# Optimization experiments

Measured on AMD Instinct MI355X. Metric: run time of the kernel, lower is better.

The kernel has to match this reference:

```python
import jax, jax.numpy as jnp
import numpy as np
import math

B, T, DIN, DOUT, D, L, H = 32, 512, 263, 263, 1024, 8, 16
EPS = 1e-5


def layer_norm(x, g, b):
    mu = jnp.mean(x, axis=-1, keepdims=True)
    var = jnp.var(x, axis=-1, keepdims=True)
    return (x - mu) * jax.lax.rsqrt(var + EPS) * g + b


def setup_inputs() -> dict:
    key = jax.random.key(0)
    ks = jax.random.split(key, 12)
    s = 0.02
    return {
        "x": jax.random.normal(ks[0], (B, T, DIN), jnp.float32),
        "src_mask": jnp.ones((B, T, T), jnp.bool_),
        "seq_emb": jax.random.normal(ks[1], (T, D), jnp.float32),  # sequence_embedding[:T]
        "joint_w": jax.random.normal(ks[2], (D, DIN), jnp.float32) * s,
        "joint_b": jnp.zeros((D,), jnp.float32),
        "ln_g": jnp.ones((L, D), jnp.float32),
        "ln_b": jnp.zeros((L, D), jnp.float32),
        "q_w": jax.random.normal(ks[3], (L, D, D), jnp.float32) * s,
        "q_b": jnp.zeros((L, D), jnp.float32),
        "k_w": jax.random.normal(ks[4], (L, D, D), jnp.float32) * s,
        "k_b": jnp.zeros((L, D), jnp.float32),
        "v_w": jax.random.normal(ks[5], (L, D, D), jnp.float32) * s,
        "v_b": jnp.zeros((L, D), jnp.float32),
        "p_w": jax.random.normal(ks[6], (L, D, D), jnp.float32) * s,
        "p_b": jnp.zeros((L, D), jnp.float32),
        "out_ln_g": jnp.ones((D,), jnp.float32),
        "out_ln_b": jnp.zeros((D,), jnp.float32),
        "out_w": jax.random.normal(ks[7], (DOUT, D), jnp.float32) * s,  # zero_module in ckpt; random here for non-degenerate baseline
        "out_b": jnp.zeros((DOUT,), jnp.float32),
    }


def reference(x, src_mask, seq_emb, joint_w, joint_b, ln_g, ln_b,
              q_w, q_b, k_w, k_b, v_w, v_b, p_w, p_b,
              out_ln_g, out_ln_b, out_w, out_b):
    Bc, Tc, _ = x.shape
    h = x @ joint_w.T + joint_b + seq_emb[None, :Tc, :]  # [B,T,D]
    neg = (1.0 - src_mask.astype(h.dtype))[..., None] * -100000.0  # [B,T,T,1]
    scale = 1.0 / math.sqrt(D // H)
    for i in range(L):
        n = layer_norm(h, ln_g[i], ln_b[i])
        q = (n @ q_w[i].T + q_b[i]).reshape(Bc, Tc, H, D // H)
        k = (n @ k_w[i].T + k_b[i]).reshape(Bc, Tc, H, D // H)
        v = (n @ v_w[i].T + v_b[i]).reshape(Bc, Tc, H, D // H)
        att = jnp.einsum('bnhd,bmhd->bnmh', q, k) * scale + neg
        w = jax.nn.softmax(att, axis=2)  # softmax over keys (m)
        y = jnp.einsum('bnmh,bmhd->bnhd', w, v).reshape(Bc, Tc, D)
        h = h + y @ p_w[i].T + p_b[i]
    return layer_norm(h, out_ln_g, out_ln_b) @ out_w.T + out_b
```

## Files before the change

### kernel.cpp

```cpp
#include <hip/hip_runtime.h>
#include <hip/hip_bf16.h>


typedef unsigned short u16;
typedef unsigned int u32;
typedef __attribute__((ext_vector_type(8))) __bf16 bf16x8;
typedef __attribute__((ext_vector_type(4))) float floatx4;
typedef __attribute__((ext_vector_type(4))) _Float16 halfx4;
typedef __attribute__((ext_vector_type(8))) _Float16 halfx8;

#define TB 512
#define DB 1024
#define F32_ONE 0x3F800000u
#define ATTN_SCALE 0.18033688f

__device__ __forceinline__ float bf2f(u16 u) { union { u32 i; float f; } c; c.i = ((u32)u) << 16; return c.f; }
__device__ __forceinline__ u16 f2bf(float f) {
  union { float f; u32 i; } c; c.f = f;
  return (u16)((c.i + 0x7fffu + ((c.i >> 16) & 1u)) >> 16);
}
__device__ __forceinline__ u32 pk_f16(float a, float b) {
  auto h = __builtin_amdgcn_cvt_pkrtz(a, b);
  union { decltype(h) v; u32 u; } c;
  c.v = h;
  return c.u;
}

__device__ __forceinline__ void gload16(const u16* g, u16* l) {
  __builtin_amdgcn_global_load_lds((const __attribute__((address_space(1))) void*)g,
                                   (__attribute__((address_space(3))) void*)l, 16, 0, 0);
}

__device__ __forceinline__ floatx4 mfma_pv(u32 p0, u32 p1, halfx4 vf, floatx4 c) {
#if __has_builtin(__builtin_amdgcn_mfma_f32_16x16x16f16)
  union { u32 u[2]; halfx4 h; } a; a.u[0] = p0; a.u[1] = p1;
  return __builtin_amdgcn_mfma_f32_16x16x16f16(a.h, vf, c, 0, 0, 0);
#else
  union { u32 u[4]; halfx8 h; } a; a.u[0] = p0; a.u[1] = p1; a.u[2] = 0; a.u[3] = 0;
  union { u32 u[4]; halfx8 h; halfx4 v4[2]; } b; b.u[2] = 0; b.u[3] = 0; b.v4[0] = vf;
  return __builtin_amdgcn_mfma_f32_16x16x32_f16(a.h, b.h, c, 0, 0, 0);
#endif
}

__global__ void cvt_bf16(const void* __restrict__ src, unsigned long long soff,
                         u16* __restrict__ dst, int rows_src, int cols_src,
                         int rows_dst, int cols_dst, const u32* __restrict__ det) {
  const bool isf = (det[0] == F32_ONE);
  const int idx = blockIdx.x * 256 + threadIdx.x;
  if (idx >= rows_dst * cols_dst) return;
  const int r = idx / cols_dst, c = idx - r * cols_dst;
  u16 v = 0;
  if (r < rows_src && c < cols_src) {
    const unsigned long long si = soff + (unsigned long long)r * cols_src + c;
    v = isf ? f2bf(((const float*)src)[si]) : ((const u16*)src)[si];
  }
  dst[idx] = v;
}

__global__ void cvt_f32(const void* __restrict__ src, float* __restrict__ dst,
                        int n_src, int n_dst, const u32* __restrict__ det) {
  const bool isf = (det[0] == F32_ONE);
  const int idx = blockIdx.x * 256 + threadIdx.x;
  if (idx >= n_dst) return;
  float v = 0.f;
  if (idx < n_src) v = isf ? ((const float*)src)[idx] : bf2f(((const u16*)src)[idx]);
  dst[idx] = v;
}

__global__ void cvt_wqkvp(const void* __restrict__ qw, const void* __restrict__ kw,
                          const void* __restrict__ vw, const void* __restrict__ pw,
                          unsigned long long woff, u16* __restrict__ dst,
                          const u32* __restrict__ det) {
  const bool isf = (det[0] == F32_ONE);
  const int idx = blockIdx.x * 256 + threadIdx.x;
  const int t = idx >> 20;
  const unsigned long long si = woff + (unsigned long long)(idx & 1048575);
  const void* src = (t == 0) ? qw : (t == 1) ? kw : (t == 2) ? vw : pw;
  dst[idx] = isf ? f2bf(((const float*)src)[si]) : ((const u16*)src)[si];
}

struct SmallTab {
  const void* src[10];
  float* dst[10];
  int nsrc[10];
  int ndst[10];
  int blk0[11];
};
__global__ void cvt_small(SmallTab tab, const u32* __restrict__ det) {
  const bool isf = (det[0] == F32_ONE);
  int s = 0;
  while (s < 9 && (int)blockIdx.x >= tab.blk0[s + 1]) ++s;
  const int idx = ((int)blockIdx.x - tab.blk0[s]) * 256 + threadIdx.x;
  if (idx >= tab.ndst[s]) return;
  float v = 0.f;
  if (idx < tab.nsrc[s])
    v = isf ? ((const float*)tab.src[s])[idx] : bf2f(((const u16*)tab.src[s])[idx]);
  tab.dst[s][idx] = v;
}

template <int MODE>
__global__ __launch_bounds__(256, 2) void gemm_bt(
    const u16* __restrict__ A, const u16* __restrict__ W,
    const float* __restrict__ bias, const float* __restrict__ bias2,
    const float* __restrict__ bias3,
    int M, int N, int K, int nbx,
    u16* __restrict__ Cbf, u16* __restrict__ Vtb, float* __restrict__ Hres,
    const float* __restrict__ seqf, void* __restrict__ Cout, int Ncol,
    const u32* __restrict__ det) {
  __shared__ u16 As[4096];
  __shared__ u16 Bs[4096];
  const int tid = threadIdx.x;
  const int lane = tid & 63;
  const int w = tid >> 6;

  const int nby = (int)gridDim.x / nbx;
  const int sby = nby >> 3;
  const int xcd = blockIdx.x & 7;
  const int lid = blockIdx.x >> 3;
  const int by = xcd * sby + (lid % sby);
  const int bx = lid / sby;
  const int m0 = by << 7;
  const int n0 = bx << 7;

  const int wm = (w >> 1) << 6;
  const int wn = (w & 1) << 6;

  const int srow = (w << 5) + (lane >> 2);
  const int koff = (lane & 3) << 3;
  const u16* Ag0 = A + (size_t)(m0 + srow) * K + koff;
  const u16* Ag1 = A + (size_t)(m0 + srow + 16) * K + koff;
  const u16* Wg0 = W + (size_t)(n0 + srow) * K + koff;
  const u16* Wg1 = W + (size_t)(n0 + srow + 16) * K + koff;
  u16* AsB0 = As + (w << 10);
  u16* AsB1 = AsB0 + 512;
  u16* BsB0 = Bs + (w << 10);
  u16* BsB1 = BsB0 + 512;

  floatx4 acc[4][4];
  floatx4 zz = {0.f, 0.f, 0.f, 0.f};
#pragma unroll
  for (int i = 0; i < 4; ++i)
#pragma unroll
    for (int j = 0; j < 4; ++j) acc[i][j] = zz;

  const int fr = lane & 15;
  const int fq = (lane >> 4) << 3;

  for (int k0 = 0; k0 < K; k0 += 32) {
    __syncthreads();
    gload16(Ag0 + k0, AsB0);
    gload16(Ag1 + k0, AsB1);
    gload16(Wg0 + k0, BsB0);
    gload16(Wg1 + k0, BsB1);
    __syncthreads();
    bf16x8 af[4], bfv[4];
#pragma unroll
    for (int i = 0; i < 4; ++i) af[i] = *(const bf16x8*)(As + ((wm + (i << 4) + fr) << 5) + fq);
#pragma unroll
    for (int j = 0; j < 4; ++j) bfv[j] = *(const bf16x8*)(Bs + ((wn + (j << 4) + fr) << 5) + fq);
#pragma unroll
    for (int i = 0; i < 4; ++i)
#pragma unroll
      for (int j = 0; j < 4; ++j)
        acc[i][j] = __builtin_amdgcn_mfma_f32_16x16x32_bf16(af[i], bfv[j], acc[i][j], 0, 0, 0);
  }

  const int er = (lane >> 4) << 2;
  const int ec = lane & 15;
  bool isf = true;
  if (MODE == 3) isf = (det[0] == F32_ONE);

#pragma unroll
  for (int i = 0; i < 4; ++i) {
#pragma unroll
    for (int j = 0; j < 4; ++j) {
      const int col = n0 + wn + (j << 4) + ec;
#pragma unroll
      for (int r = 0; r < 4; ++r) {
        const int row = m0 + wm + (i << 4) + er + r;
        float vv = acc[i][j][r];
        if (MODE == 1) {
          vv += bias[col];
          Hres[(size_t)row * N + col] += vv;
        } else if (MODE == 2) {
          vv += bias[col] + seqf[(size_t)(row & (TB - 1)) * N + col];
          Hres[(size_t)row * N + col] = vv;
        } else if (MODE == 3) {
          if (col < Ncol) {
            vv += bias[col];
            if (isf) ((float*)Cout)[(size_t)row * Ncol + col] = vv;
            else ((u16*)Cout)[(size_t)row * Ncol + col] = f2bf(vv);
          }
        }
      }
    }
  }
}


#define LGKM(n) asm volatile("s_waitcnt lgkmcnt(" #n ")" ::: "memory")

#define STAGE_A(t, h)                                                        \
  do {                                                                       \
    u16* slot_ = sh + (((t) & 1) << 15) + ((h) << 13) + (w << 9);            \
    gload16(pA[h][0] + ((t) << 6), slot_);                                   \
    gload16(pA[h][1] + ((t) << 6), slot_ + 4096);                            \
  } while (0)
#define STAGE_B(t, h)                                                        \
  do {                                                                       \
    u16* slot_ = sh + (((t) & 1) << 15) + 16384 + ((h) << 13) + (w << 9);    \
    gload16(pB[h][0] + ((t) << 6), slot_);                                   \
    gload16(pB[h][1] + ((t) << 6), slot_ + 4096);                            \
  } while (0)

#define LDA4P(DST, IG0)                                                       \
  do {                                                                        \
    _Pragma("unroll") for (int i_ = 0; i_ < 4; ++i_) {                        \
      DST[i_][0] = *(const bf16x8*)(sh + aB0 + (((IG0) + i_) << 10));         \
      DST[i_][1] = *(const bf16x8*)(sh + aB1 + (((IG0) + i_) << 10));         \
    }                                                                         \
  } while (0)
#define LDB2P(DST, JG0)                                                       \
  do {                                                                        \
    _Pragma("unroll") for (int j_ = 0; j_ < 2; ++j_) {                        \
      DST[j_][0] = *(const bf16x8*)(sh + bB0 + (((JG0) + j_) << 10));         \
      DST[j_][1] = *(const bf16x8*)(sh + bB1 + (((JG0) + j_) << 10));         \
    }                                                                         \
  } while (0)
#define MFMA16(I0, J0, AF, BB)                                                \
  do {                                                                        \
    __builtin_amdgcn_s_setprio(1);                                            \
    _Pragma("unroll") for (int i_ = 0; i_ < 4; ++i_) {                        \
      _Pragma("unroll") for (int j_ = 0; j_ < 2; ++j_) {                      \
        _Pragma("unroll") for (int ks_ = 0; ks_ < 2; ++ks_) {                 \
          acc[(I0) + i_][(J0) + j_] = __builtin_amdgcn_mfma_f32_16x16x32_bf16(\
              AF[i_][ks_], BB[j_][ks_], acc[(I0) + i_][(J0) + j_], 0, 0, 0);  \
        }                                                                     \
      }                                                                       \
    }                                                                         \
    __builtin_amdgcn_s_setprio(0);                                            \
  } while (0)

template <int MODE>
__global__ __launch_bounds__(512, 1) void gemm256_bt(
    const u16* __restrict__ A, const u16* __restrict__ W,
    const float* __restrict__ bias, const float* __restrict__ bias2,
    const float* __restrict__ bias3,
    int M, int N, int K, int nbx,
    u16* __restrict__ Cbf, u16* __restrict__ Vtb, float* __restrict__ Hres,
    const u32* __restrict__ det) {
  __shared__ u16 sh[65536];
  const int tid = threadIdx.x;
  const int lane = tid & 63;
  const int w = tid >> 6;

  const int nby = (int)gridDim.x / nbx;
  const int sby = nby >> 3;
  const int xcd = blockIdx.x & 7;
  const int lid = blockIdx.x >> 3;
  const int by = xcd * sby + (lid % sby);
  const int bx = lid / sby;
  const int m0 = by << 8;
  const int n0 = bx << 8;

  const int wmh = w >> 2;
  const int wnq = w & 3;
  const int wnh = wnq >> 1;
  const int wn1 = wnq & 1;

  const int fr = lane & 15;
  const int q4 = (lane >> 4) << 3;
  const int axor = (fr & 7) << 3;
  const int koff0 = q4 ^ axor;
  const int koff1 = (32 + q4) ^ axor;

  int aB0 = (wmh << 13) + (fr << 6) + koff0;
  int aB1 = (wmh << 13) + (fr << 6) + koff1;
  int bB0 = 16384 + (wnh << 13) + (wn1 << 12) + (fr << 6) + koff0;
  int bB1 = 16384 + (wnh << 13) + (wn1 << 12) + (fr << 6) + koff1;

  const int srow = (w << 3) + (lane >> 3);
  const int kbs2 = (((lane & 7) ^ (lane >> 3)) << 3);
  const u16* pA[2][2];
  const u16* pB[2][2];
#pragma unroll
  for (int h = 0; h < 2; ++h)
#pragma unroll
    for (int j = 0; j < 2; ++j) {
      pA[h][j] = A + (size_t)(m0 + (h << 7) + (j << 6) + srow) * K + kbs2;
      pB[h][j] = W + (size_t)(n0 + (h << 7) + (j << 6) + srow) * K + kbs2;
    }

  floatx4 acc[8][4];
  floatx4 zz = {0.f, 0.f, 0.f, 0.f};
#pragma unroll
  for (int i = 0; i < 8; ++i)
#pragma unroll
    for (int j = 0; j < 4; ++j) acc[i][j] = zz;

  STAGE_A(0, 0);
  STAGE_A(0, 1);
  STAGE_B(0, 0);
  STAGE_B(0, 1);
  STAGE_B(1, 0);
  STAGE_B(1, 1);
  asm volatile("s_waitcnt vmcnt(4)" ::: "memory");
  __builtin_amdgcn_s_barrier();

  bf16x8 afX[4][2], afY[4][2], b0[2][2], b1[2][2];
  const int NT = K >> 6;

  LDA4P(afX, 0);
  LDB2P(b0, 0);
  for (int t = 0; t < NT; ++t) {
    LDB2P(b1, 2);
    if (t + 1 < NT) STAGE_A(t + 1, 0);
    LGKM(4);
    MFMA16(0, 0, afX, b0);
    LDA4P(afY, 4);
    if (t + 1 < NT) STAGE_A(t + 1, 1);
    LGKM(8);
    MFMA16(0, 2, afX, b1);
    __builtin_amdgcn_s_barrier();
    if (t + 2 < NT) STAGE_B(t + 2, 0);
    LGKM(0);
    MFMA16(4, 0, afY, b0);
    if (t + 2 < NT) {
      STAGE_B(t + 2, 1);
      asm volatile("s_waitcnt vmcnt(4)" ::: "memory");
    } else {
      asm volatile("s_waitcnt vmcnt(0)" ::: "memory");
    }
    __builtin_amdgcn_s_barrier();
    aB0 ^= 32768; aB1 ^= 32768; bB0 ^= 32768; bB1 ^= 32768;
    if (t + 1 < NT) {
      LDA4P(afX, 0);
      LDB2P(b0, 0);
    }
    MFMA16(4, 2, afY, b1);
  }

  const int er = (lane >> 4) << 2;
  const int ec = lane & 15;

  if (MODE == 5 && n0 >= 2048) {
    const int colp0 = n0 - 2048;
    const int key0 = m0 & 511;
    const int bb = m0 >> 9;
#pragma unroll
    for (int p = 0; p < 2; ++p) {
      __syncthreads();
      if (wnh == p) {
#pragma unroll
        for (int i = 0; i < 8; ++i)
#pragma unroll
          for (int j = 0; j < 4; ++j) {
            const int c = (wn1 << 6) + (j << 4) + ec;
            const float bv = bias3[colp0 + (p << 7) + c];
            const int keyl = (wmh << 7) + (i << 4) + er;
            uint2 pk2;
            pk2.x = pk_f16(acc[i][j][0] + bv, acc[i][j][1] + bv);
            pk2.y = pk_f16(acc[i][j][2] + bv, acc[i][j][3] + bv);
            *(uint2*)&sh[c * 264 + keyl] = pk2;
          }
      }
      __syncthreads();
#pragma unroll
      for (int it = 0; it < 8; ++it) {
        const int idx = (it << 9) + tid;
        const int c = idx >> 5;
        const int ch = idx & 31;
        const int colp = colp0 + (p << 7) + c;
        u16* dst = Vtb + ((((size_t)((bb << 4) | (colp >> 6)) << 6) | (colp & 63)) << 9) +
                   key0 + (ch << 3);
        *(uint4*)dst = *(const uint4*)&sh[c * 264 + (ch << 3)];
      }
    }
    return;
  }

#pragma unroll
  for (int i = 0; i < 8; ++i) {
#pragma unroll
    for (int j = 0; j < 4; ++j) {
      const int col = n0 + (wnq << 6) + (j << 4) + ec;
      if (MODE == 5) {
        const float bv = (col < 1024) ? bias[col] : bias2[col - 1024];
#pragma unroll
        for (int r = 0; r < 4; ++r) {
          const int row = m0 + (wmh << 7) + (i << 4) + er + r;
          Cbf[(size_t)row * 2048 + col] = f2bf(acc[i][j][r] + bv);
        }
      } else if (MODE == 1) {
        const float bv = bias[col];
#pragma unroll
        for (int r = 0; r < 4; ++r) {
          const int row = m0 + (wmh << 7) + (i << 4) + er + r;
          Hres[(size_t)row * N + col] += acc[i][j][r] + bv;
        }
      }
    }
  }
}

__global__ __launch_bounds__(256, 4) void ln_kernel(const float* __restrict__ h,
                                                    const float* __restrict__ g,
                                                    const float* __restrict__ b,
                                                    u16* __restrict__ outp) {
  const int w = threadIdx.x >> 6, lane = threadIdx.x & 63;
  const int row = (blockIdx.x << 2) + w;
  const float4* hr = (const float4*)(h + (size_t)row * DB);
  float4 xv[4];
  float s = 0.f, ss = 0.f;
#pragma unroll
  for (int k = 0; k < 4; ++k) {
    xv[k] = hr[lane + (k << 6)];
    s += (xv[k].x + xv[k].y) + (xv[k].z + xv[k].w);
    ss += (xv[k].x * xv[k].x + xv[k].y * xv[k].y) + (xv[k].z * xv[k].z + xv[k].w * xv[k].w);
  }
#pragma unroll
  for (int o = 32; o > 0; o >>= 1) {
    s += __shfl_xor(s, o);
    ss += __shfl_xor(ss, o);
  }
  const float mu = s * (1.f / 1024.f);
  const float var = ss * (1.f / 1024.f) - mu * mu;
  const float rstd = rsqrtf(var + 1e-5f);
  u32* orow = (u32*)(outp + (size_t)row * DB);
#pragma unroll
  for (int k = 0; k < 4; ++k) {
    const float4 gv = ((const float4*)g)[lane + (k << 6)];
    const float4 bv = ((const float4*)b)[lane + (k << 6)];
    const float y0 = (xv[k].x - mu) * rstd * gv.x + bv.x;
    const float y1 = (xv[k].y - mu) * rstd * gv.y + bv.y;
    const float y2 = (xv[k].z - mu) * rstd * gv.z + bv.z;
    const float y3 = (xv[k].w - mu) * rstd * gv.w + bv.w;
    orow[((lane + (k << 6)) << 1)] = (u32)f2bf(y0) | ((u32)f2bf(y1) << 16);
    orow[((lane + (k << 6)) << 1) + 1] = (u32)f2bf(y2) | ((u32)f2bf(y3) << 16);
  }
}

__global__ __launch_bounds__(256, 3) void attn_mfma(const u16* __restrict__ qkg,
                                                    const u16* __restrict__ vtg,
                                                    u16* __restrict__ yg) {
  __shared__ u16 Ks[2][4096];
  __shared__ u16 Vt[2][4096];
  const int tid = threadIdx.x;
  const int lane = tid & 63;
  const int w = tid >> 6;
  const int bh = blockIdx.x;
  const int b = bh >> 4, h = bh & 15;
  const int q0 = blockIdx.y << 7;
  const int ln15 = lane & 15;
  const int quad = lane >> 4;
  const int l7 = ln15 & 7;
  const int r8 = lane >> 3;
  const int swc = ((lane & 7) ^ r8) << 3;

  bf16x8 qa[2][2];
#pragma unroll
  for (int g = 0; g < 2; ++g) {
    const size_t qrow = (size_t)(b * TB + q0 + w * 32 + g * 16 + ln15) * 2048 + h * 64;
#pragma unroll
    for (int ks = 0; ks < 2; ++ks) {
      union { bf16x8 v; u16 u[8]; } c;
      c.v = *(const bf16x8*)(qkg + qrow + ks * 32 + quad * 8);
#pragma unroll
      for (int j = 0; j < 8; ++j) c.u[j] = f2bf(bf2f(c.u[j]) * ATTN_SCALE);
      qa[g][ks] = c.v;
    }
  }

  const u16* kgb = qkg + 1024 + h * 64;
  const u16* vgb = vtg + ((size_t)bh << 15);

  floatx4 o4[2][4];
  floatx4 zz = {0.f, 0.f, 0.f, 0.f};
#pragma unroll
  for (int g = 0; g < 2; ++g)
#pragma unroll
    for (int n = 0; n < 4; ++n) o4[g][n] = zz;
  float lsum[2] = {0.f, 0.f};

  const int rl0 = w * 16 + r8;
  auto issue = [&](int t, int buf) {
    const int kt = t << 6;
#pragma unroll
    for (int i = 0; i < 2; ++i) {
      const int rloc = rl0 + i * 8;
      gload16(kgb + (size_t)(b * TB + kt + rloc) * 2048 + swc, &Ks[buf][(w << 10) + (i << 9)]);
      gload16(vgb + ((size_t)rloc << 9) + kt + swc, &Vt[buf][(w << 10) + (i << 9)]);
    }
  };

  issue(0, 0);
  for (int t = 0; t < 8; ++t) {
    const int buf = t & 1;
    __syncthreads();
    if (t < 7) issue(t + 1, buf ^ 1);

    bf16x8 kf[2][4];
#pragma unroll
    for (int ks = 0; ks < 2; ++ks)
#pragma unroll
      for (int n = 0; n < 4; ++n)
        kf[ks][n] = *(const bf16x8*)(&Ks[buf][(((n << 4) | ln15) << 6) +
                                             ((((ks << 2) | quad) ^ l7) << 3)]);
    floatx4 s4[2][4];
#pragma unroll
    for (int g = 0; g < 2; ++g)
#pragma unroll
      for (int n = 0; n < 4; ++n) s4[g][n] = zz;
    __builtin_amdgcn_s_setprio(1);
#pragma unroll
    for (int ks = 0; ks < 2; ++ks)
#pragma unroll
      for (int n = 0; n < 4; ++n) {
        s4[0][n] = __builtin_amdgcn_mfma_f32_16x16x32_bf16(kf[ks][n], qa[0][ks], s4[0][n], 0, 0, 0);
        s4[1][n] = __builtin_amdgcn_mfma_f32_16x16x32_bf16(kf[ks][n], qa[1][ks], s4[1][n], 0, 0, 0);
      }
    __builtin_amdgcn_s_setprio(0);

    u32 pa[2][4][2];
#pragma unroll
    for (int g = 0; g < 2; ++g)
#pragma unroll
      for (int n = 0; n < 4; ++n) {
        const float p0 = exp2f(s4[g][n][0]);
        const float p1 = exp2f(s4[g][n][1]);
        const float p2 = exp2f(s4[g][n][2]);
        const float p3 = exp2f(s4[g][n][3]);
        lsum[g] += (p0 + p1) + (p2 + p3);
        pa[g][n][0] = pk_f16(p0, p1);
        pa[g][n][1] = pk_f16(p2, p3);
      }

    __builtin_amdgcn_s_setprio(1);
#pragma unroll
    for (int kt16 = 0; kt16 < 4; ++kt16) {
#pragma unroll
      for (int n = 0; n < 4; ++n) {
        halfx4 vf = *(const halfx4*)(&Vt[buf][(((n << 4) | ln15) << 6) +
                                             ((((kt16 << 1) | (quad >> 1)) ^ l7) << 3) +
                                             ((quad & 1) << 2)]);
        o4[0][n] = mfma_pv(pa[0][kt16][0], pa[0][kt16][1], vf, o4[0][n]);
        o4[1][n] = mfma_pv(pa[1][kt16][0], pa[1][kt16][1], vf, o4[1][n]);
      }
    }
    __builtin_amdgcn_s_setprio(0);
  }

#pragma unroll
  for (int g = 0; g < 2; ++g) {
    float lf = lsum[g];
    lf += __shfl_xor(lf, 16);
    lf += __shfl_xor(lf, 32);
#pragma unroll
    for (int r = 0; r < 4; ++r) {
      const float linv = 1.0f / __shfl(lf, (quad << 4) + (quad << 2) + r, 64);
      const size_t yr = (size_t)(b * TB + q0 + w * 32 + g * 16 + (quad << 2) + r) * DB + h * 64;
#pragma unroll
      for (int n = 0; n < 4; ++n) yg[yr + (n << 4) + ln15] = f2bf(o4[g][n][r] * linv);
    }
  }
}

extern "C" void kernel_launch(void* const* d_in, const int* in_sizes, int n_in,
                              void* d_out, int out_size, void* d_ws, size_t ws_size,
                              hipStream_t stream) {
  const void* x = d_in[0];
  const void* seq = d_in[2];
  const void* jw = d_in[3];
  const void* jb = d_in[4];
  const void* lng = d_in[5];
  const void* lnb = d_in[6];
  const void* qw = d_in[7];
  const void* qbias = d_in[8];
  const void* kw = d_in[9];
  const void* kbias = d_in[10];
  const void* vw = d_in[11];
  const void* vbias = d_in[12];
  const void* pw = d_in[13];
  const void* pbias = d_in[14];
  const void* olng = d_in[15];
  const void* olnb = d_in[16];
  const void* ow = d_in[17];
  const void* ob = d_in[18];
  const u32* det = (const u32*)lng;

  char* ws = (char*)d_ws;
  float* h = (float*)ws;
  u16* nbuf = (u16*)(ws + 67108864);
  u16* qk = (u16*)(ws + 100663296);
  u16* vt = (u16*)(ws + 167772160);
  u16* ybuf = (u16*)(ws + 201326592);
  u16* xpad = ybuf;
  u16* wcvt = (u16*)(ws + 234881024);
  u16* jwpad = (u16*)(ws + 243269632);
  u16* owpad = (u16*)(ws + 243859456);
  float* seqf = (float*)(ws + 244645888);
  float* smallf = (float*)(ws + 246743040);
  float* jbf = smallf;
  float* lngf = smallf + 1024;
  float* lnbf = smallf + 9216;
  float* qbf = smallf + 17408;
  float* kbf = smallf + 25600;
  float* vbf = smallf + 33792;
  float* pbf = smallf + 41984;
  float* olngf = smallf + 50176;
  float* olnbf = smallf + 51200;
  float* obf = smallf + 52224;

  cvt_bf16<<<dim3(16384 * 288 / 256), 256, 0, stream>>>(x, 0ull, xpad, 16384, 263, 16384, 288, det);
  cvt_bf16<<<dim3(1024 * 288 / 256), 256, 0, stream>>>(jw, 0ull, jwpad, 1024, 263, 1024, 288, det);
  cvt_bf16<<<dim3(384 * 1024 / 256), 256, 0, stream>>>(ow, 0ull, owpad, 263, 1024, 384, 1024, det);
  cvt_f32<<<dim3(2048), 256, 0, stream>>>(seq, seqf, 512 * 1024, 512 * 1024, det);
  {
    SmallTab tab;
    const void* srcs[10] = {jb, lng, lnb, qbias, kbias, vbias, pbias, olng, olnb, ob};
    float* dsts[10] = {jbf, lngf, lnbf, qbf, kbf, vbf, pbf, olngf, olnbf, obf};
    const int ns[10] = {1024, 8192, 8192, 8192, 8192, 8192, 8192, 1024, 1024, 263};
    const int nd[10] = {1024, 8192, 8192, 8192, 8192, 8192, 8192, 1024, 1024, 384};
    int acc = 0;
    for (int i = 0; i < 10; ++i) {
      tab.src[i] = srcs[i]; tab.dst[i] = dsts[i]; tab.nsrc[i] = ns[i]; tab.ndst[i] = nd[i];
      tab.blk0[i] = acc; acc += (nd[i] + 255) / 256;
    }
    tab.blk0[10] = acc;
    cvt_small<<<dim3(acc), 256, 0, stream>>>(tab, det);
  }

  gemm_bt<2><<<dim3(1024), 256, 0, stream>>>(xpad, jwpad, jbf, nullptr, nullptr,
                                             16384, 1024, 288, 8, nullptr, nullptr, h, seqf,
                                             nullptr, 0, det);

  for (int i = 0; i < 8; ++i) {
    const unsigned long long woff = (unsigned long long)i * 1048576ull;
    cvt_wqkvp<<<dim3(16384), 256, 0, stream>>>(qw, kw, vw, pw, woff, wcvt, det);
    ln_kernel<<<dim3(4096), 256, 0, stream>>>(h, lngf + i * 1024, lnbf + i * 1024, nbuf);
    gemm256_bt<5><<<dim3(768), 512, 0, stream>>>(nbuf, wcvt, qbf + i * 1024, kbf + i * 1024,
                                                 vbf + i * 1024, 16384, 3072, 1024, 12,
                                                 qk, vt, nullptr, det);
    attn_mfma<<<dim3(512, 4), 256, 0, stream>>>(qk, vt, ybuf);
    gemm256_bt<1><<<dim3(256), 512, 0, stream>>>(ybuf, wcvt + 3145728, pbf + i * 1024, nullptr,
                                                 nullptr, 16384, 1024, 1024, 4,
                                                 nullptr, nullptr, h, det);
  }

  ln_kernel<<<dim3(4096), 256, 0, stream>>>(h, olngf, olnbf, nbuf);
  gemm_bt<3><<<dim3(384), 256, 0, stream>>>(nbuf, owpad, obf, nullptr, nullptr,
                                            16384, 384, 1024, 3, nullptr, nullptr, nullptr,
                                            nullptr, d_out, 263, det);
}
```

Measured before the change: 2.246 ms.

## Triple-buffer B tiles in LDS to drop a per-iteration barrier

Moves the B operand staging from a double buffer to a three-slot ring in shared memory, with A kept double-buffered in a compacted region. The extra slot means the prefetch of B for tile t+2 no longer overwrites data still being read, so the mid-iteration barrier before issuing that prefetch is removed. LDS use grows from 128KB to 160KB per block, and the ring offsets are updated with per-iteration rotation arithmetic.

```diff
diff --git a/kernel.cpp b/kernel.cpp
--- a/kernel.cpp
+++ b/kernel.cpp
@@ -202,13 +202,13 @@
 
 #define STAGE_A(t, h)                                                        \
   do {                                                                       \
-    u16* slot_ = sh + (((t) & 1) << 15) + ((h) << 13) + (w << 9);            \
+    u16* slot_ = sh + (((t) & 1) << 14) + ((h) << 13) + (w << 9);            \
     gload16(pA[h][0] + ((t) << 6), slot_);                                   \
     gload16(pA[h][1] + ((t) << 6), slot_ + 4096);                            \
   } while (0)
-#define STAGE_B(t, h)                                                        \
+#define STAGE_B(t, OFF, h)                                                   \
   do {                                                                       \
-    u16* slot_ = sh + (((t) & 1) << 15) + 16384 + ((h) << 13) + (w << 9);    \
+    u16* slot_ = sh + 32768 + (OFF) + ((h) << 13) + (w << 9);                \
     gload16(pB[h][0] + ((t) << 6), slot_);                                   \
     gload16(pB[h][1] + ((t) << 6), slot_ + 4096);                            \
   } while (0)
@@ -223,8 +223,8 @@
 #define LDB2P(DST, JG0)                                                       \
   do {                                                                        \
     _Pragma("unroll") for (int j_ = 0; j_ < 2; ++j_) {                        \
-      DST[j_][0] = *(const bf16x8*)(sh + bB0 + (((JG0) + j_) << 10));         \
-      DST[j_][1] = *(const bf16x8*)(sh + bB1 + (((JG0) + j_) << 10));         \
+      DST[j_][0] = *(const bf16x8*)(sh + bR0 + (((JG0) + j_) << 10));         \
+      DST[j_][1] = *(const bf16x8*)(sh + bR1 + (((JG0) + j_) << 10));         \
     }                                                                         \
   } while (0)
 #define MFMA16(I0, J0, AF, BB)                                                \
@@ -249,7 +249,7 @@
     int M, int N, int K, int nbx,
     u16* __restrict__ Cbf, u16* __restrict__ Vtb, float* __restrict__ Hres,
     const u32* __restrict__ det) {
-  __shared__ u16 sh[65536];
+  __shared__ u16 sh[81920];
   const int tid = threadIdx.x;
   const int lane = tid & 63;
   const int w = tid >> 6;
@@ -276,8 +276,11 @@
 
   int aB0 = (wmh << 13) + (fr << 6) + koff0;
   int aB1 = (wmh << 13) + (fr << 6) + koff1;
-  int bB0 = 16384 + (wnh << 13) + (wn1 << 12) + (fr << 6) + koff0;
-  int bB1 = 16384 + (wnh << 13) + (wn1 << 12) + (fr << 6) + koff1;
+  const int bC0 = 32768 + (wnh << 13) + (wn1 << 12) + (fr << 6) + koff0;
+  const int bC1 = 32768 + (wnh << 13) + (wn1 << 12) + (fr << 6) + koff1;
+  int bOff = 0;
+  int sOff = 32768;
+  int bR0 = bC0, bR1 = bC1;
 
   const int srow = (w << 3) + (lane >> 3);
   const int kbs2 = (((lane & 7) ^ (lane >> 3)) << 3);
@@ -300,10 +303,10 @@
 
   STAGE_A(0, 0);
   STAGE_A(0, 1);
-  STAGE_B(0, 0);
-  STAGE_B(0, 1);
-  STAGE_B(1, 0);
-  STAGE_B(1, 1);
+  STAGE_B(0, 0, 0);
+  STAGE_B(0, 0, 1);
+  STAGE_B(1, 16384, 0);
+  STAGE_B(1, 16384, 1);
   asm volatile("s_waitcnt vmcnt(4)" ::: "memory");
   __builtin_amdgcn_s_barrier();
 
@@ -321,18 +324,20 @@
     if (t + 1 < NT) STAGE_A(t + 1, 1);
     LGKM(8);
     MFMA16(0, 2, afX, b1);
-    __builtin_amdgcn_s_barrier();
-    if (t + 2 < NT) STAGE_B(t + 2, 0);
+    if (t + 2 < NT) STAGE_B(t + 2, sOff, 0);
     LGKM(0);
     MFMA16(4, 0, afY, b0);
     if (t + 2 < NT) {
-      STAGE_B(t + 2, 1);
+      STAGE_B(t + 2, sOff, 1);
       asm volatile("s_waitcnt vmcnt(4)" ::: "memory");
     } else {
       asm volatile("s_waitcnt vmcnt(0)" ::: "memory");
     }
     __builtin_amdgcn_s_barrier();
-    aB0 ^= 32768; aB1 ^= 32768; bB0 ^= 32768; bB1 ^= 32768;
+    aB0 ^= 16384; aB1 ^= 16384;
+    bOff = (bOff == 32768) ? 0 : bOff + 16384;
+    sOff = (sOff == 32768) ? 0 : sOff + 16384;
+    bR0 = bC0 + bOff; bR1 = bC1 + bOff;
     if (t + 1 < NT) {
       LDA4P(afX, 0);
       LDB2P(b0, 0);
```

Result: no change. 2.214 ms (-1.4%).
